# Kernel optimization log

Measured on AMD Instinct MI355X. Metric: run time of the kernel, lower is better.

The kernel has to match this reference:

```python
import jax, jax.numpy as jnp
import numpy as np

B, T, C = 2, 2048, 1024
N_HEAD = 16
HEAD_DIM = C // N_HEAD


def setup_inputs() -> dict:
    key = jax.random.key(0)
    k1, k2, k3 = jax.random.split(key, 3)
    x = jax.random.normal(k1, (B, T, C), dtype=jnp.float32)
    # weights stored as [in, out]; torch Linear computes x @ W.T with weight [out, in]
    W_qkv = jax.random.normal(k2, (C, 3 * C), dtype=jnp.float32) * (1.0 / np.sqrt(C))
    W_proj = jax.random.normal(k3, (C, C), dtype=jnp.float32) * (1.0 / np.sqrt(C))
    return {"x": x, "W_qkv": W_qkv, "W_proj": W_proj}


def reference(x, W_qkv, W_proj):
    Bb, Tt, Cc = x.shape
    qkv = x @ W_qkv                                # [B,T,3C]
    q, k, v = jnp.split(qkv, 3, axis=2)
    # [B,T,H,D] -> [B,H,T,D]
    q = q.reshape(Bb, Tt, N_HEAD, HEAD_DIM).transpose(0, 2, 1, 3)
    k = k.reshape(Bb, Tt, N_HEAD, HEAD_DIM).transpose(0, 2, 1, 3)
    v = v.reshape(Bb, Tt, N_HEAD, HEAD_DIM).transpose(0, 2, 1, 3)
    scale = 1.0 / np.sqrt(HEAD_DIM).astype(np.float32)
    att = jnp.einsum('bhqd,bhkd->bhqk', q, k) * scale   # [B,H,T,T]
    causal = jnp.tril(jnp.ones((Tt, Tt), dtype=bool))
    att = jnp.where(causal[None, None], att, -jnp.inf)
    att = jax.nn.softmax(att, axis=-1)
    y = jnp.einsum('bhqk,bhkd->bhqd', att, v)           # [B,H,T,D]
    y = y.transpose(0, 2, 1, 3).reshape(Bb, Tt, Cc)
    return y @ W_proj
```

## Files before the change

### kernel.cpp

```cpp
#include <hip/hip_runtime.h>
#include <hip/hip_bf16.h>
#include <math.h>


typedef __bf16 bf16_t;
typedef __bf16 bf16x4 __attribute__((ext_vector_type(4)));
typedef __bf16 bf16x8 __attribute__((ext_vector_type(8)));
typedef float  f32x4  __attribute__((ext_vector_type(4)));

#define MFMA16(a, b, c) __builtin_amdgcn_mfma_f32_16x16x32_bf16((a), (b), (c), 0, 0, 0)

#define Bn 2
#define Tn 2048
#define Cn 1024
#define Hn 16
#define Dn 64
#define C3 3072
#define Mn 4096
#define QKW 2048
#define NEG_BIG (-1e30f)
#define SCL2 0.18033688011112042f
#define M2   17.31234049066756f

__device__ __forceinline__ void gload_lds16(const void* g, void* l) {
    __builtin_amdgcn_global_load_lds(
        (const __attribute__((address_space(1))) unsigned int*)g,
        (__attribute__((address_space(3))) unsigned int*)l, 16, 0, 0);
}

__device__ __forceinline__ bf16x8 cat44(bf16x4 a, bf16x4 b) {
    bf16x8 r;
    r[0] = a[0]; r[1] = a[1]; r[2] = a[2]; r[3] = a[3];
    r[4] = b[0]; r[5] = b[1]; r[6] = b[2]; r[7] = b[3];
    return r;
}

__global__ __launch_bounds__(256) void transpose_cvt(const float* __restrict__ in,
                                                     bf16_t* __restrict__ out,
                                                     int K, int N) {
    __shared__ float tile[32][33];
    int n0 = blockIdx.x * 32, k0 = blockIdx.y * 32;
    int tx = threadIdx.x, ty = threadIdx.y;
#pragma unroll
    for (int i = 0; i < 32; i += 8)
        tile[ty + i][tx] = in[(size_t)(k0 + ty + i) * N + n0 + tx];
    __syncthreads();
#pragma unroll
    for (int i = 0; i < 32; i += 8)
        out[(size_t)(n0 + ty + i) * K + k0 + tx] = (bf16_t)tile[tx][ty + i];
}

__global__ __launch_bounds__(256) void transpose_v(const bf16_t* __restrict__ in,
                                                   bf16_t* __restrict__ out) {
    __shared__ bf16_t tile[32][34];
    int c0 = blockIdx.x * 32;
    int t0 = blockIdx.y * 32;
    int b  = blockIdx.z;
    const bf16_t* ib = in  + (size_t)b * Tn * Cn;
    bf16_t* ob       = out + (size_t)b * Cn * Tn;
    int tx = threadIdx.x, ty = threadIdx.y;
#pragma unroll
    for (int i = 0; i < 32; i += 8)
        tile[ty + i][tx] = ib[(size_t)(t0 + ty + i) * Cn + c0 + tx];
    __syncthreads();
#pragma unroll
    for (int i = 0; i < 32; i += 8)
        ob[(size_t)(c0 + ty + i) * Tn + t0 + tx] = tile[tx][ty + i];
}

__global__ __launch_bounds__(256) void cvt_bf16(const float* __restrict__ in,
                                                bf16_t* __restrict__ out) {
    size_t i = ((size_t)blockIdx.x * 256 + threadIdx.x) * 8;
    f32x4 a = *(const f32x4*)(in + i);
    f32x4 b = *(const f32x4*)(in + i + 4);
    bf16x8 r;
    r[0] = (bf16_t)a[0]; r[1] = (bf16_t)a[1]; r[2] = (bf16_t)a[2]; r[3] = (bf16_t)a[3];
    r[4] = (bf16_t)b[0]; r[5] = (bf16_t)b[1]; r[6] = (bf16_t)b[2]; r[7] = (bf16_t)b[3];
    *(bf16x8*)(out + i) = r;
}

template <typename AT, typename CT, int MODE>
__global__ __launch_bounds__(256) void gemm_m97(const AT* __restrict__ A, int lda,
                                                const bf16_t* __restrict__ BT,
                                                CT* __restrict__ Cout, int ldc, int Kd,
                                                bf16_t* __restrict__ qk,
                                                bf16_t* __restrict__ vT) {
    constexpr bool AF32 = (sizeof(AT) == 4);
    __shared__ AT     As[128 * 32];
    __shared__ bf16_t Bs[128 * 32];

    const int tid = threadIdx.x;
    const int w = tid >> 6, lane = tid & 63;
    const int l16 = lane & 15, quad = lane >> 4;
    const int wm = w & 1, wn = w >> 1;
    const int n0 = blockIdx.x * 128;
    const int m0 = blockIdx.y * 128;

    f32x4 zero = {0.f, 0.f, 0.f, 0.f};
    f32x4 acc[4][4];
#pragma unroll
    for (int mb = 0; mb < 4; mb++)
#pragma unroll
        for (int nb = 0; nb < 4; nb++) acc[mb][nb] = zero;

    for (int k = 0; k < Kd; k += 32) {
        __syncthreads();
        if (AF32) {
#pragma unroll
            for (int j = 0; j < 4; j++) {
                int seg = w * 4 + j;
                int r = seg * 8 + (lane >> 3);
                int cc = (lane & 7) ^ (r & 7);
                const float* g = (const float*)A + (size_t)(m0 + r) * lda + k + cc * 4;
                gload_lds16(g, (char*)As + seg * 1024);
            }
        } else {
#pragma unroll
            for (int j = 0; j < 2; j++) {
                int seg = w * 2 + j;
                int r = seg * 16 + (lane >> 2);
                int cc = (lane & 3) ^ (r & 3);
                const bf16_t* g = (const bf16_t*)A + (size_t)(m0 + r) * lda + k + cc * 8;
                gload_lds16(g, (char*)As + seg * 1024);
            }
        }
#pragma unroll
        for (int j = 0; j < 2; j++) {
            int seg = w * 2 + j;
            int r = seg * 16 + (lane >> 2);
            int cc = (lane & 3) ^ (r & 3);
            const bf16_t* g = BT + (size_t)(n0 + r) * Kd + k + cc * 8;
            gload_lds16(g, (char*)Bs + seg * 1024);
        }
        __syncthreads();

        bf16x8 af[4], bf[4];
#pragma unroll
        for (int mb = 0; mb < 4; mb++) {
            int r = wm * 64 + mb * 16 + l16;
            if (AF32) {
                f32x4 x0 = *(const f32x4*)((const char*)As + (r * 8 + ((quad * 2) ^ (r & 7))) * 16);
                f32x4 x1 = *(const f32x4*)((const char*)As + (r * 8 + ((quad * 2 + 1) ^ (r & 7))) * 16);
                bf16x8 t;
                t[0] = (bf16_t)x0[0]; t[1] = (bf16_t)x0[1]; t[2] = (bf16_t)x0[2]; t[3] = (bf16_t)x0[3];
                t[4] = (bf16_t)x1[0]; t[5] = (bf16_t)x1[1]; t[6] = (bf16_t)x1[2]; t[7] = (bf16_t)x1[3];
                af[mb] = t;
            } else {
                af[mb] = *(const bf16x8*)((const char*)As + (r * 4 + (quad ^ (r & 3))) * 16);
            }
        }
#pragma unroll
        for (int nb = 0; nb < 4; nb++) {
            int r = wn * 64 + nb * 16 + l16;
            bf[nb] = *(const bf16x8*)((const char*)Bs + (r * 4 + (quad ^ (r & 3))) * 16);
        }
#pragma unroll
        for (int mb = 0; mb < 4; mb++)
#pragma unroll
            for (int nb = 0; nb < 4; nb++)
                acc[mb][nb] = MFMA16(af[mb], bf[nb], acc[mb][nb]);
    }

#pragma unroll
    for (int mb = 0; mb < 4; mb++)
#pragma unroll
        for (int nb = 0; nb < 4; nb++) {
            const int col = n0 + wn * 64 + nb * 16 + l16;
            const int row0 = m0 + wm * 64 + mb * 16 + quad * 4;
            if (MODE == 0) {
#pragma unroll
                for (int rr = 0; rr < 4; rr++)
                    Cout[(size_t)(row0 + rr) * ldc + col] = (CT)acc[mb][nb][rr];
            } else {
                if (col < 2048) {
#pragma unroll
                    for (int rr = 0; rr < 4; rr++)
                        qk[(size_t)(row0 + rr) * QKW + col] = (bf16_t)acc[mb][nb][rr];
                } else if (MODE == 2) {
                    int hcol = col - 2048;
#pragma unroll
                    for (int rr = 0; rr < 4; rr++)
                        vT[(size_t)(row0 + rr) * Cn + hcol] = (bf16_t)acc[mb][nb][rr];
                } else {
                    int hcol = col - 2048;
                    int bb = row0 >> 11, t0 = row0 & 2047;
                    bf16x4 pv;
#pragma unroll
                    for (int rr = 0; rr < 4; rr++) pv[rr] = (bf16_t)acc[mb][nb][rr];
                    *(bf16x4*)(vT + ((size_t)(bb * 1024 + hcol)) * Tn + t0) = pv;
                }
            }
        }
}

__global__ __launch_bounds__(256) void gemm_s(const bf16_t* __restrict__ A, int lda,
                                              const bf16_t* __restrict__ BT,
                                              float* __restrict__ Cout, int ldc, int Kd) {
    __shared__ bf16_t As[64 * 32];
    __shared__ bf16_t Bs[128 * 32];

    const int tid = threadIdx.x;
    const int w = tid >> 6, lane = tid & 63;
    const int l16 = lane & 15, quad = lane >> 4;
    const int wm = w & 1, wn = w >> 1;
    const int n0 = blockIdx.x * 128;
    const int m0 = blockIdx.y * 64;

    f32x4 zero = {0.f, 0.f, 0.f, 0.f};
    f32x4 acc[2][4];
#pragma unroll
    for (int mb = 0; mb < 2; mb++)
#pragma unroll
        for (int nb = 0; nb < 4; nb++) acc[mb][nb] = zero;

    for (int k = 0; k < Kd; k += 32) {
        __syncthreads();
        {
            int r = w * 16 + (lane >> 2);
            int cc = (lane & 3) ^ (r & 3);
            const bf16_t* g = A + (size_t)(m0 + r) * lda + k + cc * 8;
            gload_lds16(g, (char*)As + w * 1024);
        }
#pragma unroll
        for (int j = 0; j < 2; j++) {
            int seg = w * 2 + j;
            int r = seg * 16 + (lane >> 2);
            int cc = (lane & 3) ^ (r & 3);
            const bf16_t* g = BT + (size_t)(n0 + r) * Kd + k + cc * 8;
            gload_lds16(g, (char*)Bs + seg * 1024);
        }
        __syncthreads();

        bf16x8 af[2], bf[4];
#pragma unroll
        for (int mb = 0; mb < 2; mb++) {
            int r = wm * 32 + mb * 16 + l16;
            af[mb] = *(const bf16x8*)((const char*)As + (r * 4 + (quad ^ (r & 3))) * 16);
        }
#pragma unroll
        for (int nb = 0; nb < 4; nb++) {
            int r = wn * 64 + nb * 16 + l16;
            bf[nb] = *(const bf16x8*)((const char*)Bs + (r * 4 + (quad ^ (r & 3))) * 16);
        }
#pragma unroll
        for (int mb = 0; mb < 2; mb++)
#pragma unroll
            for (int nb = 0; nb < 4; nb++)
                acc[mb][nb] = MFMA16(af[mb], bf[nb], acc[mb][nb]);
    }

#pragma unroll
    for (int mb = 0; mb < 2; mb++)
#pragma unroll
        for (int nb = 0; nb < 4; nb++) {
            const int col = n0 + wn * 64 + nb * 16 + l16;
            const int row0 = m0 + wm * 32 + mb * 16 + quad * 4;
#pragma unroll
            for (int rr = 0; rr < 4; rr++)
                Cout[(size_t)(row0 + rr) * ldc + col] = acc[mb][nb][rr];
        }
}

__global__ __launch_bounds__(256) void attn_kernel(bf16_t* __restrict__ qk,
                                                   const bf16_t* __restrict__ vT) {
    const int id = blockIdx.x;
    const int bh = id & 31;
    const int pr = id >> 5;
    const int b = bh >> 4, h = bh & 15;
    const int tA = pr;
    const int tB = 31 - pr;
    const int tmax = tB;

    const int tid = threadIdx.x;
    const int wave = tid >> 6, lane = tid & 63;
    const int l16 = lane & 15, quad = lane >> 4;

    __shared__ __align__(16) bf16_t Kb[3][64 * 64];
    __shared__ __align__(16) bf16_t Vb[3][64 * 64];

    bf16_t* qbase = qk + (size_t)b * Tn * QKW + h * Dn;
    const bf16_t* kbase = qk + (size_t)b * Tn * QKW + Cn + h * Dn;
    const bf16_t* vbase = vT + (size_t)(b * 1024 + h * Dn) * Tn;

    const int qA = tA * 64 + wave * 16;
    const int qB = tB * 64 + wave * 16;

    bf16x8 qfA[2], qfB[2];
#pragma unroll
    for (int ks = 0; ks < 2; ks++) {
        qfA[ks] = *(const bf16x8*)(qbase + (size_t)(qA + l16) * QKW + ks * 32 + quad * 8);
        qfB[ks] = *(const bf16x8*)(qbase + (size_t)(qB + l16) * QKW + ks * 32 + quad * 8);
    }

    bf16x8 ones;
#pragma unroll
    for (int j = 0; j < 8; j++) ones[j] = (bf16_t)1.0f;

    f32x4 zero = {0.f, 0.f, 0.f, 0.f};
    f32x4 oA[4], oB[4];
    f32x4 olA, olB;
#pragma unroll
    for (int i = 0; i < 4; i++) { oA[i] = zero; oB[i] = zero; }
    olA = zero; olB = zero;

    const int r8 = lane >> 3;
    const int cc = (lane & 7) ^ r8;
    auto STAGE = [&](int t, int pg) {
        const int key0 = t * 64;
#pragma unroll
        for (int j = 0; j < 2; j++) {
            int seg = wave * 2 + j;
            gload_lds16(kbase + (size_t)(key0 + seg * 8 + r8) * QKW + cc * 8,
                        (char*)&Kb[pg][0] + seg * 1024);
            gload_lds16(vbase + (size_t)(seg * 8 + r8) * Tn + key0 + cc * 8,
                        (char*)&Vb[pg][0] + seg * 1024);
        }
    };

    STAGE(0, 0);
    STAGE(1, 1);
    int cur = 0;

    for (int t = 0; t <= tmax; ++t) {
        asm volatile("s_waitcnt vmcnt(4)" ::: "memory");
        __builtin_amdgcn_sched_barrier(0);
        __builtin_amdgcn_s_barrier();
        __builtin_amdgcn_sched_barrier(0);
        if (t + 2 <= tmax) {
            int st = cur + 2; if (st >= 3) st -= 3;
            STAGE(t + 2, st);
        }
        __builtin_amdgcn_sched_barrier(0);

        const bool shp = (t <= tA);
        const char* Kc = (const char*)&Kb[cur][0];
        const char* Vc = (const char*)&Vb[cur][0];

        bf16x8 kf[2][4];
#pragma unroll
        for (int ks = 0; ks < 2; ks++)
#pragma unroll
            for (int nbk = 0; nbk < 4; nbk++) {
                int R = nbk * 16 + l16;
                kf[ks][nbk] = *(const bf16x8*)(Kc + R * 128 +
                                               (((ks * 4 + quad) ^ (R & 7)) << 4));
            }

        bf16x4 pkA[4], pkB[4];

        {
            f32x4 sx[4];
#pragma unroll
            for (int nbk = 0; nbk < 4; nbk++) sx[nbk] = zero;
            __builtin_amdgcn_s_setprio(1);
#pragma unroll
            for (int nbk = 0; nbk < 4; nbk++) {
                sx[nbk] = MFMA16(kf[0][nbk], qfB[0], sx[nbk]);
                sx[nbk] = MFMA16(kf[1][nbk], qfB[1], sx[nbk]);
            }
            __builtin_amdgcn_s_setprio(0);
            if (t == tB) {
                int q = qB + l16;
#pragma unroll
                for (int nbk = 0; nbk < 4; nbk++)
#pragma unroll
                    for (int r = 0; r < 4; r++) {
                        int key = t * 64 + nbk * 16 + quad * 4 + r;
                        if (key > q) sx[nbk][r] = NEG_BIG;
                    }
            }
#pragma unroll
            for (int nbk = 0; nbk < 4; nbk++)
#pragma unroll
                for (int r = 0; r < 4; r++)
                    pkB[nbk][r] = (bf16_t)__builtin_exp2f(__builtin_fmaf(sx[nbk][r], SCL2, -M2));
        }

        if (shp) {
            f32x4 sx[4];
#pragma unroll
            for (int nbk = 0; nbk < 4; nbk++) sx[nbk] = zero;
            __builtin_amdgcn_s_setprio(1);
#pragma unroll
            for (int nbk = 0; nbk < 4; nbk++) {
                sx[nbk] = MFMA16(kf[0][nbk], qfA[0], sx[nbk]);
                sx[nbk] = MFMA16(kf[1][nbk], qfA[1], sx[nbk]);
            }
            __builtin_amdgcn_s_setprio(0);
            if (t == tA) {
                int q = qA + l16;
#pragma unroll
                for (int nbk = 0; nbk < 4; nbk++)
#pragma unroll
                    for (int r = 0; r < 4; r++) {
                        int key = t * 64 + nbk * 16 + quad * 4 + r;
                        if (key > q) sx[nbk][r] = NEG_BIG;
                    }
            }
#pragma unroll
            for (int nbk = 0; nbk < 4; nbk++)
#pragma unroll
                for (int r = 0; r < 4; r++)
                    pkA[nbk][r] = (bf16_t)__builtin_exp2f(__builtin_fmaf(sx[nbk][r], SCL2, -M2));
        } else {
#pragma unroll
            for (int nbk = 0; nbk < 4; nbk++)
#pragma unroll
                for (int r = 0; r < 4; r++) pkA[nbk][r] = (bf16_t)0.0f;
        }

        const int gl = quad >> 1, sub = (quad & 1) * 8;
        __builtin_amdgcn_s_setprio(1);
#pragma unroll
        for (int ks = 0; ks < 2; ks++) {
            bf16x8 pfB_ = cat44(pkB[2 * ks], pkB[2 * ks + 1]);
            bf16x8 pfA_ = cat44(pkA[2 * ks], pkA[2 * ks + 1]);
#pragma unroll
            for (int nbd = 0; nbd < 4; nbd++) {
                int R = nbd * 16 + l16, r7 = R & 7;
                const char* row = Vc + R * 128;
                bf16x4 lo = *(const bf16x4*)(row + (((ks * 4 + gl) ^ r7) << 4) + sub);
                bf16x4 hi = *(const bf16x4*)(row + (((ks * 4 + 2 + gl) ^ r7) << 4) + sub);
                bf16x8 vf = cat44(lo, hi);
                oB[nbd] = MFMA16(pfB_, vf, oB[nbd]);
                if (shp) oA[nbd] = MFMA16(pfA_, vf, oA[nbd]);
            }
            olB = MFMA16(pfB_, ones, olB);
            if (shp) olA = MFMA16(pfA_, ones, olA);
        }
        __builtin_amdgcn_s_setprio(0);

        cur = cur + 1; if (cur >= 3) cur -= 3;
    }

#pragma unroll
    for (int nbd = 0; nbd < 4; nbd++)
#pragma unroll
        for (int r = 0; r < 4; r++) {
            int ta = qA + quad * 4 + r;
            int tb = qB + quad * 4 + r;
            qbase[(size_t)ta * QKW + nbd * 16 + l16] = (bf16_t)(oA[nbd][r] / olA[r]);
            qbase[(size_t)tb * QKW + nbd * 16 + l16] = (bf16_t)(oB[nbd][r] / olB[r]);
        }
}

extern "C" void kernel_launch(void* const* d_in, const int* in_sizes, int n_in,
                              void* d_out, int out_size, void* d_ws, size_t ws_size,
                              hipStream_t stream) {
    const float* x     = (const float*)d_in[0];
    const float* Wqkv  = (const float*)d_in[1];
    const float* Wproj = (const float*)d_in[2];
    float* out = (float*)d_out;

    bf16_t* qk     = (bf16_t*)d_ws;
    bf16_t* vslot  = qk + (size_t)Mn * QKW;
    bf16_t* wqkvT  = vslot + (size_t)QKW * Tn;
    bf16_t* wprojT = wqkvT + (size_t)C3 * Cn;
    bf16_t* xb     = wprojT + (size_t)Cn * Cn;

    const size_t NEED_XB = ((size_t)Mn * QKW + (size_t)QKW * Tn + (size_t)C3 * Cn +
                            (size_t)Cn * Cn + (size_t)Mn * Cn) * sizeof(bf16_t);

    transpose_cvt<<<dim3(C3 / 32, Cn / 32), dim3(32, 8), 0, stream>>>(Wqkv, wqkvT, Cn, C3);
    transpose_cvt<<<dim3(Cn / 32, Cn / 32), dim3(32, 8), 0, stream>>>(Wproj, wprojT, Cn, Cn);

    if (ws_size >= NEED_XB) {
        cvt_bf16<<<dim3((Mn * Cn) / 2048), 256, 0, stream>>>(x, xb);
        gemm_m97<bf16_t, bf16_t, 2><<<dim3(C3 / 128, Mn / 128), 256, 0, stream>>>(
            xb, Cn, wqkvT, (bf16_t*)nullptr, 0, Cn, qk, vslot);
        transpose_v<<<dim3(Cn / 32, Tn / 32, Bn), dim3(32, 8), 0, stream>>>(vslot, xb);
        attn_kernel<<<dim3(512), 256, 0, stream>>>(qk, xb);
    } else {
        gemm_m97<float, bf16_t, 1><<<dim3(C3 / 128, Mn / 128), 256, 0, stream>>>(
            x, Cn, wqkvT, (bf16_t*)nullptr, 0, Cn, qk, vslot);
        attn_kernel<<<dim3(512), 256, 0, stream>>>(qk, vslot);
    }
    gemm_s<<<dim3(Cn / 128, Mn / 64), 256, 0, stream>>>(qk, QKW, wprojT, out, Cn, Cn);
}
```

Before: 197.9 us.

## Fuse V transpose into QKV GEMM, prescale Q, and pack softmax probabilities

The QKV GEMM now writes V directly in transposed layout for the bf16 path, removing the separate transpose kernel and its extra global memory pass. Q is pre-multiplied by the log2 softmax scale in the GEMM epilogue, so attention uses a bare hardware exp2 without a per-element FMA or fixed offset. Probabilities are converted with packed bf16 conversion instructions, and LDS swizzle offsets are precomputed outside the key loop. Dropping the fixed offset reduces headroom against exp overflow for large scores, and the transposed V store in the GEMM epilogue writes short strided vectors.

```diff
diff --git a/kernel.cpp b/kernel.cpp
--- a/kernel.cpp
+++ b/kernel.cpp
@@ -7,6 +7,7 @@
 typedef __bf16 bf16x4 __attribute__((ext_vector_type(4)));
 typedef __bf16 bf16x8 __attribute__((ext_vector_type(8)));
 typedef float  f32x4  __attribute__((ext_vector_type(4)));
+typedef unsigned int u32x4 __attribute__((ext_vector_type(4)));
 
 #define MFMA16(a, b, c) __builtin_amdgcn_mfma_f32_16x16x32_bf16((a), (b), (c), 0, 0, 0)
 
@@ -20,7 +21,6 @@
 #define QKW 2048
 #define NEG_BIG (-1e30f)
 #define SCL2 0.18033688011112042f
-#define M2   17.31234049066756f
 
 __device__ __forceinline__ void gload_lds16(const void* g, void* l) {
     __builtin_amdgcn_global_load_lds(
@@ -28,10 +28,9 @@
         (__attribute__((address_space(3))) unsigned int*)l, 16, 0, 0);
 }
 
-__device__ __forceinline__ bf16x8 cat44(bf16x4 a, bf16x4 b) {
-    bf16x8 r;
-    r[0] = a[0]; r[1] = a[1]; r[2] = a[2]; r[3] = a[3];
-    r[4] = b[0]; r[5] = b[1]; r[6] = b[2]; r[7] = b[3];
+__device__ __forceinline__ unsigned cvtpk_bf16(float a, float b) {
+    unsigned r;
+    asm("v_cvt_pk_bf16_f32 %0, %1, %2" : "=v"(r) : "v"(a), "v"(b));
     return r;
 }
 
@@ -48,24 +47,6 @@
 #pragma unroll
     for (int i = 0; i < 32; i += 8)
         out[(size_t)(n0 + ty + i) * K + k0 + tx] = (bf16_t)tile[tx][ty + i];
-}
-
-__global__ __launch_bounds__(256) void transpose_v(const bf16_t* __restrict__ in,
-                                                   bf16_t* __restrict__ out) {
-    __shared__ bf16_t tile[32][34];
-    int c0 = blockIdx.x * 32;
-    int t0 = blockIdx.y * 32;
-    int b  = blockIdx.z;
-    const bf16_t* ib = in  + (size_t)b * Tn * Cn;
-    bf16_t* ob       = out + (size_t)b * Cn * Tn;
-    int tx = threadIdx.x, ty = threadIdx.y;
-#pragma unroll
-    for (int i = 0; i < 32; i += 8)
-        tile[ty + i][tx] = ib[(size_t)(t0 + ty + i) * Cn + c0 + tx];
-    __syncthreads();
-#pragma unroll
-    for (int i = 0; i < 32; i += 8)
-        ob[(size_t)(c0 + ty + i) * Tn + t0 + tx] = tile[tx][ty + i];
 }
 
 __global__ __launch_bounds__(256) void cvt_bf16(const float* __restrict__ in,
@@ -173,14 +154,10 @@
                     Cout[(size_t)(row0 + rr) * ldc + col] = (CT)acc[mb][nb][rr];
             } else {
                 if (col < 2048) {
+                    const float sc = (col < 1024) ? SCL2 : 1.0f;
 #pragma unroll
                     for (int rr = 0; rr < 4; rr++)
-                        qk[(size_t)(row0 + rr) * QKW + col] = (bf16_t)acc[mb][nb][rr];
-                } else if (MODE == 2) {
-                    int hcol = col - 2048;
-#pragma unroll
-                    for (int rr = 0; rr < 4; rr++)
-                        vT[(size_t)(row0 + rr) * Cn + hcol] = (bf16_t)acc[mb][nb][rr];
+                        qk[(size_t)(row0 + rr) * QKW + col] = (bf16_t)(acc[mb][nb][rr] * sc);
                 } else {
                     int hcol = col - 2048;
                     int bb = row0 >> 11, t0 = row0 & 2047;
@@ -303,6 +280,18 @@
     for (int i = 0; i < 4; i++) { oA[i] = zero; oB[i] = zero; }
     olA = zero; olB = zero;
 
+    const int gl = quad >> 1, sub = (quad & 1) * 8;
+    int kOff[2][4], vLo[2][4], vHi[2][4];
+#pragma unroll
+    for (int ks = 0; ks < 2; ks++)
+#pragma unroll
+        for (int nb = 0; nb < 4; nb++) {
+            int R = nb * 16 + l16, r7 = R & 7;
+            kOff[ks][nb] = R * 128 + (((ks * 4 + quad) ^ r7) << 4);
+            vLo[ks][nb]  = R * 128 + (((ks * 4 + gl) ^ r7) << 4) + sub;
+            vHi[ks][nb]  = R * 128 + (((ks * 4 + 2 + gl) ^ r7) << 4) + sub;
+        }
+
     const int r8 = lane >> 3;
     const int cc = (lane & 7) ^ r8;
     auto STAGE = [&](int t, int pg) {
@@ -340,13 +329,10 @@
 #pragma unroll
         for (int ks = 0; ks < 2; ks++)
 #pragma unroll
-            for (int nbk = 0; nbk < 4; nbk++) {
-                int R = nbk * 16 + l16;
-                kf[ks][nbk] = *(const bf16x8*)(Kc + R * 128 +
-                                               (((ks * 4 + quad) ^ (R & 7)) << 4));
-            }
-
-        bf16x4 pkA[4], pkB[4];
+            for (int nbk = 0; nbk < 4; nbk++)
+                kf[ks][nbk] = *(const bf16x8*)(Kc + kOff[ks][nbk]);
+
+        bf16x8 pfA[2], pfB[2];
 
         {
             f32x4 sx[4];
@@ -373,7 +359,16 @@
             for (int nbk = 0; nbk < 4; nbk++)
 #pragma unroll
                 for (int r = 0; r < 4; r++)
-                    pkB[nbk][r] = (bf16_t)__builtin_exp2f(__builtin_fmaf(sx[nbk][r], SCL2, -M2));
+                    sx[nbk][r] = __builtin_amdgcn_exp2f(sx[nbk][r]);
+#pragma unroll
+            for (int ks = 0; ks < 2; ks++) {
+                u32x4 wds;
+                wds.x = cvtpk_bf16(sx[2 * ks][0], sx[2 * ks][1]);
+                wds.y = cvtpk_bf16(sx[2 * ks][2], sx[2 * ks][3]);
+                wds.z = cvtpk_bf16(sx[2 * ks + 1][0], sx[2 * ks + 1][1]);
+                wds.w = cvtpk_bf16(sx[2 * ks + 1][2], sx[2 * ks + 1][3]);
+                pfB[ks] = __builtin_bit_cast(bf16x8, wds);
+            }
         }
 
         if (shp) {
@@ -401,32 +396,37 @@
             for (int nbk = 0; nbk < 4; nbk++)
 #pragma unroll
                 for (int r = 0; r < 4; r++)
-                    pkA[nbk][r] = (bf16_t)__builtin_exp2f(__builtin_fmaf(sx[nbk][r], SCL2, -M2));
+                    sx[nbk][r] = __builtin_amdgcn_exp2f(sx[nbk][r]);
+#pragma unroll
+            for (int ks = 0; ks < 2; ks++) {
+                u32x4 wds;
+                wds.x = cvtpk_bf16(sx[2 * ks][0], sx[2 * ks][1]);
+                wds.y = cvtpk_bf16(sx[2 * ks][2], sx[2 * ks][3]);
+                wds.z = cvtpk_bf16(sx[2 * ks + 1][0], sx[2 * ks + 1][1]);
+                wds.w = cvtpk_bf16(sx[2 * ks + 1][2], sx[2 * ks + 1][3]);
+                pfA[ks] = __builtin_bit_cast(bf16x8, wds);
+            }
         } else {
-#pragma unroll
-            for (int nbk = 0; nbk < 4; nbk++)
-#pragma unroll
-                for (int r = 0; r < 4; r++) pkA[nbk][r] = (bf16_t)0.0f;
-        }
-
-        const int gl = quad >> 1, sub = (quad & 1) * 8;
+            u32x4 z = {0u, 0u, 0u, 0u};
+            pfA[0] = __builtin_bit_cast(bf16x8, z);
+            pfA[1] = __builtin_bit_cast(bf16x8, z);
+        }
+
         __builtin_amdgcn_s_setprio(1);
 #pragma unroll
         for (int ks = 0; ks < 2; ks++) {
-            bf16x8 pfB_ = cat44(pkB[2 * ks], pkB[2 * ks + 1]);
-            bf16x8 pfA_ = cat44(pkA[2 * ks], pkA[2 * ks + 1]);
 #pragma unroll
             for (int nbd = 0; nbd < 4; nbd++) {
-                int R = nbd * 16 + l16, r7 = R & 7;
-                const char* row = Vc + R * 128;
-                bf16x4 lo = *(const bf16x4*)(row + (((ks * 4 + gl) ^ r7) << 4) + sub);
-                bf16x4 hi = *(const bf16x4*)(row + (((ks * 4 + 2 + gl) ^ r7) << 4) + sub);
-                bf16x8 vf = cat44(lo, hi);
-                oB[nbd] = MFMA16(pfB_, vf, oB[nbd]);
-                if (shp) oA[nbd] = MFMA16(pfA_, vf, oA[nbd]);
-            }
-            olB = MFMA16(pfB_, ones, olB);
-            if (shp) olA = MFMA16(pfA_, ones, olA);
+                bf16x4 lo = *(const bf16x4*)(Vc + vLo[ks][nbd]);
+                bf16x4 hi = *(const bf16x4*)(Vc + vHi[ks][nbd]);
+                bf16x8 vf;
+                vf[0] = lo[0]; vf[1] = lo[1]; vf[2] = lo[2]; vf[3] = lo[3];
+                vf[4] = hi[0]; vf[5] = hi[1]; vf[6] = hi[2]; vf[7] = hi[3];
+                oB[nbd] = MFMA16(pfB[ks], vf, oB[nbd]);
+                if (shp) oA[nbd] = MFMA16(pfA[ks], vf, oA[nbd]);
+            }
+            olB = MFMA16(pfB[ks], ones, olB);
+            if (shp) olA = MFMA16(pfA[ks], ones, olA);
         }
         __builtin_amdgcn_s_setprio(0);
 
@@ -453,8 +453,8 @@
     float* out = (float*)d_out;
 
     bf16_t* qk     = (bf16_t*)d_ws;
-    bf16_t* vslot  = qk + (size_t)Mn * QKW;
-    bf16_t* wqkvT  = vslot + (size_t)QKW * Tn;
+    bf16_t* vT     = qk + (size_t)Mn * QKW;
+    bf16_t* wqkvT  = vT + (size_t)QKW * Tn;
     bf16_t* wprojT = wqkvT + (size_t)C3 * Cn;
     bf16_t* xb     = wprojT + (size_t)Cn * Cn;
 
@@ -466,14 +466,12 @@
 
     if (ws_size >= NEED_XB) {
         cvt_bf16<<<dim3((Mn * Cn) / 2048), 256, 0, stream>>>(x, xb);
-        gemm_m97<bf16_t, bf16_t, 2><<<dim3(C3 / 128, Mn / 128), 256, 0, stream>>>(
-            xb, Cn, wqkvT, (bf16_t*)nullptr, 0, Cn, qk, vslot);
-        transpose_v<<<dim3(Cn / 32, Tn / 32, Bn), dim3(32, 8), 0, stream>>>(vslot, xb);
-        attn_kernel<<<dim3(512), 256, 0, stream>>>(qk, xb);
+        gemm_m97<bf16_t, bf16_t, 1><<<dim3(C3 / 128, Mn / 128), 256, 0, stream>>>(
+            xb, Cn, wqkvT, (bf16_t*)nullptr, 0, Cn, qk, vT);
     } else {
         gemm_m97<float, bf16_t, 1><<<dim3(C3 / 128, Mn / 128), 256, 0, stream>>>(
-            x, Cn, wqkvT, (bf16_t*)nullptr, 0, Cn, qk, vslot);
-        attn_kernel<<<dim3(512), 256, 0, stream>>>(qk, vslot);
+            x, Cn, wqkvT, (bf16_t*)nullptr, 0, Cn, qk, vT);
     }
+    attn_kernel<<<dim3(512), 256, 0, stream>>>(qk, vT);
     gemm_s<<<dim3(Cn / 128, Mn / 64), 256, 0, stream>>>(qk, QKW, wprojT, out, Cn, Cn);
 }
```

After: 187.5 us. 1.06x faster.
